# Optimization experiments

Measured on AMD Instinct MI355X. Metric: run time of the kernel, lower is better.

## Reference

```python
import jax, jax.numpy as jnp
import numpy as np

T, B, D = 4096, 64, 64
SCALE = D ** (-0.5)


def setup_inputs() -> dict:
    key = jax.random.key(0)
    ks = jax.random.split(key, 8)
    init = 1.0 / np.sqrt(D)  # mimic nn.Linear default scale roughly
    return {
        "eeg": jax.random.normal(ks[0], (T, B, D), dtype=jnp.float32),
        "fnirs": jax.random.normal(ks[1], (T, B, D), dtype=jnp.float32),
        "Wq": jax.random.normal(ks[2], (D, D), dtype=jnp.float32) * init,
        "bq": jax.random.normal(ks[3], (D,), dtype=jnp.float32) * init,
        "Wk": jax.random.normal(ks[4], (D, D), dtype=jnp.float32) * init,
        "bk": jax.random.normal(ks[5], (D,), dtype=jnp.float32) * init,
        "Wv": jax.random.normal(ks[6], (D, D), dtype=jnp.float32) * init,
        "bv": jax.random.normal(ks[7], (D,), dtype=jnp.float32) * init,
    }


def reference(eeg, fnirs, Wq, bq, Wk, bk, Wv, bv):
    # Linear layers: x @ W.T + b (torch nn.Linear convention, W is [out, in])
    q = jnp.einsum("tbd,od->tbo", eeg, Wq) + bq      # [T, B, D]
    k = jnp.einsum("tbd,od->tbo", fnirs, Wk) + bk    # [T, B, D]
    v = jnp.einsum("tbd,od->tbo", fnirs, Wv) + bv    # [T, B, D]
    # Elementwise QK gating score, summed over feature dim -> [T, B, 1]
    score = jnp.sum(q * k, axis=-1, keepdims=True) * SCALE
    # Softmax over the sequence axis (dim=0)
    attn = jax.nn.softmax(score, axis=0)
    # Residual combine
    return eeg + attn * v
```

## Files before the change

### kernel.cpp

```cpp
#include <hip/hip_runtime.h>
#include <hip/hip_bf16.h>
#include <math.h>

#define T_DIM 4096
#define B_DIM 64
#define NROWS (T_DIM * B_DIM)
#define NTILES (NROWS / 16)

#define WS_MFRAG 0
#define WS_VFRAG 2048
#define WS_U     4096
#define WS_W     4160
#define WS_C     4224
#define WS_MX    4240
#define WS_INV   4304
#define WS_PM    4368
#define WS_PS    8464
#define WS_SCORE 16384

typedef __attribute__((ext_vector_type(4))) float f32x4;
typedef __attribute__((ext_vector_type(8))) short bf16x8;

static __device__ inline short f2bf(float x) {
  __hip_bfloat16 h = __float2bfloat16(x);
  return *reinterpret_cast<short*>(&h);
}

static __device__ inline bf16x8 cvt8(const float4 a, const float4 b) {
  bf16x8 r;
  r[0] = f2bf(a.x); r[1] = f2bf(a.y); r[2] = f2bf(a.z); r[3] = f2bf(a.w);
  r[4] = f2bf(b.x); r[5] = f2bf(b.y); r[6] = f2bf(b.z); r[7] = f2bf(b.w);
  return r;
}

static __device__ inline float dot4(const float4 a, const float4 b, float acc) {
  acc = fmaf(a.x, b.x, acc); acc = fmaf(a.y, b.y, acc);
  acc = fmaf(a.z, b.z, acc); acc = fmaf(a.w, b.w, acc);
  return acc;
}

static __device__ __host__ inline int frag_idx(int d, int k) {
  return ((d >> 4) * 2 + (k >> 5)) * 512 +
         ((((k >> 3) & 3) * 16 + (d & 15)) * 8) + (k & 7);
}

static __device__ inline void gll16(const float* src, float* ldsbase) {
  __builtin_amdgcn_global_load_lds(
      (const __attribute__((address_space(1))) unsigned int*)src,
      (__attribute__((address_space(3))) unsigned int*)ldsbase, 16, 0, 0);
}

__global__ __launch_bounds__(64) void k1_precompute(
    const float* __restrict__ Wq, const float* __restrict__ bq,
    const float* __restrict__ Wk, const float* __restrict__ bk,
    const float* __restrict__ Wv, float* __restrict__ ws) {
  const int tid = threadIdx.x;
  const int blk = blockIdx.x;
  unsigned short* __restrict__ mfrag = (unsigned short*)(ws + WS_MFRAG);
  unsigned short* __restrict__ vfrag = (unsigned short*)(ws + WS_VFRAG);
  if (blk < 64) {
    const int d = blk;
    float acc = 0.f;
#pragma unroll
    for (int o = 0; o < 64; ++o)
      acc = fmaf(Wq[o * 64 + d], Wk[o * 64 + tid], acc);
    const int idx = frag_idx(d, tid);
    mfrag[idx] = (unsigned short)f2bf(acc);
    vfrag[idx] = (unsigned short)f2bf(Wv[d * 64 + tid]);
  } else {
    float uacc = 0.f, wacc = 0.f, cacc = 0.f;
#pragma unroll
    for (int o = 0; o < 64; ++o) {
      uacc = fmaf(bq[o], Wk[o * 64 + tid], uacc);
      wacc = fmaf(Wq[o * 64 + tid], bk[o], wacc);
      cacc = fmaf(bq[o], bk[o], cacc);
    }
    ws[WS_U + tid] = uacc;
    ws[WS_W + tid] = wacc;
    if (tid == 0) ws[WS_C] = cacc;
  }
}


#define K2_STAGE(b_, t_)                                                      \
  {                                                                           \
    const size_t rb_ = (size_t)(t_) * 16;                                     \
    float* Lb_ = &stg[wv][b_][0];                                             \
    _Pragma("unroll") for (int q = 0; q < 4; ++q)                             \
        gll16(fnirs + (rb_ + (lane & 15)) * 64 + (q * 4 + (lane >> 4)) * 4,   \
              Lb_ + q * 256);                                                 \
    _Pragma("unroll") for (int q = 0; q < 4; ++q)                             \
        gll16(eeg + (rb_ + (lane & 15)) * 64 + (q * 4 + (lane >> 4)) * 4,     \
              Lb_ + 1024 + q * 256);                                          \
  }

#define K2_COMP(b_, t_)                                                       \
  {                                                                           \
    const float* LF_ = &stg[wv][b_][0];                                       \
    const float* LE_ = &stg[wv][b_][1024];                                    \
    const float4 f0a_ = *reinterpret_cast<const float4*>(LF_ + (2 * g) * 64 + c * 4); \
    const float4 f0b_ = *reinterpret_cast<const float4*>(LF_ + (2 * g + 1) * 64 + c * 4); \
    const float4 f1a_ = *reinterpret_cast<const float4*>(LF_ + (8 + 2 * g) * 64 + c * 4); \
    const float4 f1b_ = *reinterpret_cast<const float4*>(LF_ + (9 + 2 * g) * 64 + c * 4); \
    float s_ = dot4(f0a_, u0a, dot4(f0b_, u0b, dot4(f1a_, u1a, dot4(f1b_, u1b, 0.f)))); \
    const bf16x8 a0_ = cvt8(f0a_, f0b_);                                      \
    const bf16x8 a1_ = cvt8(f1a_, f1b_);                                      \
    f32x4 acc_[4];                                                            \
    _Pragma("unroll") for (int dt = 0; dt < 4; ++dt) {                        \
      acc_[dt] = __builtin_amdgcn_mfma_f32_16x16x32_bf16(bm[dt][0], a0_, zero, 0, 0, 0); \
      acc_[dt] = __builtin_amdgcn_mfma_f32_16x16x32_bf16(bm[dt][1], a1_, acc_[dt], 0, 0, 0); \
    }                                                                         \
    _Pragma("unroll") for (int dt = 0; dt < 4; ++dt) {                        \
      const float4 Ed_ = *reinterpret_cast<const float4*>(LE_ + (dt * 4 + g) * 64 + c * 4); \
      float4 h_;                                                              \
      h_.x = acc_[dt][0] + wfr[dt].x; h_.y = acc_[dt][1] + wfr[dt].y;         \
      h_.z = acc_[dt][2] + wfr[dt].z; h_.w = acc_[dt][3] + wfr[dt].w;         \
      s_ = dot4(Ed_, h_, s_);                                                 \
    }                                                                         \
    s_ += __shfl_xor(s_, 16, 64);                                             \
    s_ += __shfl_xor(s_, 32, 64);                                             \
    if (lane < 16) score[(t_) * 16 + lane] = (s_ + cb) * 0.125f;              \
  }

__global__ __launch_bounds__(256, 2) void k2_score_mfma(
    const float* __restrict__ eeg, const float* __restrict__ fnirs,
    const float* __restrict__ wsf, float* __restrict__ score) {
  __shared__ float stg[4][2][2048];
  __shared__ unsigned short mw[4096];
  __shared__ float wl[64];

  const int tid = threadIdx.x;
  const int lane = tid & 63;
  const int wv = tid >> 6;
  const int c = lane & 15;
  const int g = lane >> 4;

  {
    const float4* msrc = reinterpret_cast<const float4*>(wsf + WS_MFRAG);
    float4* mdst = reinterpret_cast<float4*>(mw);
    mdst[tid] = msrc[tid];
    mdst[tid + 256] = msrc[tid + 256];
    if (tid < 64) wl[tid] = wsf[WS_W + tid];
  }
  __syncthreads();

  bf16x8 bm[4][2];
#pragma unroll
  for (int dt = 0; dt < 4; ++dt)
#pragma unroll
    for (int kf = 0; kf < 2; ++kf)
      bm[dt][kf] = *reinterpret_cast<const bf16x8*>(
          mw + (((dt * 2 + kf) << 9) + lane * 8));
  float4 wfr[4];
#pragma unroll
  for (int dt = 0; dt < 4; ++dt)
    wfr[dt] = *reinterpret_cast<const float4*>(&wl[dt * 16 + g * 4]);
  const float4 u0a = *reinterpret_cast<const float4*>(wsf + WS_U + g * 8);
  const float4 u0b = *reinterpret_cast<const float4*>(wsf + WS_U + g * 8 + 4);
  const float4 u1a = *reinterpret_cast<const float4*>(wsf + WS_U + 32 + g * 8);
  const float4 u1b = *reinterpret_cast<const float4*>(wsf + WS_U + 36 + g * 8);
  const float cb = wsf[WS_C];
  const f32x4 zero = {0.f, 0.f, 0.f, 0.f};

  const int t0 = (blockIdx.x * 4 + wv) * 4;

  K2_STAGE(0, t0);
  K2_STAGE(1, t0 + 1);
  asm volatile("s_waitcnt vmcnt(8)" ::: "memory");
  __builtin_amdgcn_sched_barrier(0);
  K2_COMP(0, t0);
  K2_STAGE(0, t0 + 2);
  asm volatile("s_waitcnt vmcnt(8)" ::: "memory");
  __builtin_amdgcn_sched_barrier(0);
  K2_COMP(1, t0 + 1);
  K2_STAGE(1, t0 + 3);
  asm volatile("s_waitcnt vmcnt(8)" ::: "memory");
  __builtin_amdgcn_sched_barrier(0);
  K2_COMP(0, t0 + 2);
  asm volatile("s_waitcnt vmcnt(0)" ::: "memory");
  __builtin_amdgcn_sched_barrier(0);
  K2_COMP(1, t0 + 3);
}

__global__ __launch_bounds__(256) void k3a_partial(
    const float* __restrict__ sc, float* __restrict__ pm,
    float* __restrict__ ps) {
  __shared__ float sm[4][64], ss[4][64];
  const int tid = threadIdx.x;
  const int b = tid & 63;
  const int tq = tid >> 6;
  const int t0 = blockIdx.x * 64;
  float m = -1e30f, s = 0.f;
#pragma unroll
  for (int k = 0; k < 16; ++k) {
    const float v = sc[(size_t)(t0 + k * 4 + tq) * 64 + b];
    const float mn = fmaxf(m, v);
    s = s * __expf(m - mn) + __expf(v - mn);
    m = mn;
  }
  sm[tq][b] = m; ss[tq][b] = s;
  __syncthreads();
  if (tid < 64) {
    float M = sm[0][b], S = ss[0][b];
#pragma unroll
    for (int w = 1; w < 4; ++w) {
      const float m2 = sm[w][b], s2 = ss[w][b];
      const float Mn = fmaxf(M, m2);
      S = S * __expf(M - Mn) + s2 * __expf(m2 - Mn);
      M = Mn;
    }
    pm[blockIdx.x * 64 + b] = M;
    ps[blockIdx.x * 64 + b] = S;
  }
}

__global__ __launch_bounds__(64) void k3b_combine(
    const float* __restrict__ pm, const float* __restrict__ ps,
    float* __restrict__ mx, float* __restrict__ inv) {
  const int b = threadIdx.x;
  float M = pm[b], S = ps[b];
#pragma unroll
  for (int ck = 1; ck < 64; ++ck) {
    const float m2 = pm[ck * 64 + b], s2 = ps[ck * 64 + b];
    const float Mn = fmaxf(M, m2);
    S = S * __expf(M - Mn) + s2 * __expf(m2 - Mn);
    M = Mn;
  }
  mx[b] = M;
  inv[b] = 1.0f / S;
}


#define K4_STAGE(b_, t_, scv_)                                                \
  {                                                                           \
    const size_t rb_ = (size_t)(t_) * 16;                                     \
    float* Lb_ = &stg[wv][b_][0];                                             \
    _Pragma("unroll") for (int q = 0; q < 4; ++q)                             \
        gll16(fnirs + (rb_ + (lane & 15)) * 64 + (q * 4 + (lane >> 4)) * 4,   \
              Lb_ + q * 256);                                                 \
    _Pragma("unroll") for (int q = 0; q < 4; ++q)                             \
        gll16(eeg + (rb_ + (lane & 15)) * 64 + (q * 4 + (lane >> 4)) * 4,     \
              Lb_ + 1024 + q * 256);                                          \
    scv_ = score[(t_) * 16 + c];                                              \
  }

#define K4_COMP(b_, t_, scv_)                                                 \
  {                                                                           \
    const float* LF_ = &stg[wv][b_][0];                                       \
    const float* LE_ = &stg[wv][b_][1024];                                    \
    const float4 f0a_ = *reinterpret_cast<const float4*>(LF_ + (2 * g) * 64 + c * 4); \
    const float4 f0b_ = *reinterpret_cast<const float4*>(LF_ + (2 * g + 1) * 64 + c * 4); \
    const float4 f1a_ = *reinterpret_cast<const float4*>(LF_ + (8 + 2 * g) * 64 + c * 4); \
    const float4 f1b_ = *reinterpret_cast<const float4*>(LF_ + (9 + 2 * g) * 64 + c * 4); \
    const bf16x8 a0_ = cvt8(f0a_, f0b_);                                      \
    const bf16x8 a1_ = cvt8(f1a_, f1b_);                                      \
    f32x4 acc_[4];                                                            \
    _Pragma("unroll") for (int dt = 0; dt < 4; ++dt) {                        \
      acc_[dt] = __builtin_amdgcn_mfma_f32_16x16x32_bf16(bm[dt][0], a0_, zero, 0, 0, 0); \
      acc_[dt] = __builtin_amdgcn_mfma_f32_16x16x32_bf16(bm[dt][1], a1_, acc_[dt], 0, 0, 0); \
    }                                                                         \
    const int bl_ = (((t_) * 16) & 63) + c;                                   \
    const float aC_ = __expf((scv_) - mxl[bl_]) * invl[bl_];                  \
    float* ob_ = out + ((size_t)(t_) * 16 + c) * 64;                          \
    _Pragma("unroll") for (int dt = 0; dt < 4; ++dt) {                        \
      const float4 Ed_ = *reinterpret_cast<const float4*>(LE_ + (dt * 4 + g) * 64 + c * 4); \
      float4 o_;                                                              \
      o_.x = fmaf(aC_, acc_[dt][0] + bvf[dt].x, Ed_.x);                       \
      o_.y = fmaf(aC_, acc_[dt][1] + bvf[dt].y, Ed_.y);                       \
      o_.z = fmaf(aC_, acc_[dt][2] + bvf[dt].z, Ed_.z);                       \
      o_.w = fmaf(aC_, acc_[dt][3] + bvf[dt].w, Ed_.w);                       \
      *reinterpret_cast<float4*>(ob_ + dt * 16 + g * 4) = o_;                 \
    }                                                                         \
  }

__global__ __launch_bounds__(256, 2) void k4_output_mfma(
    const float* __restrict__ eeg, const float* __restrict__ fnirs,
    const float* __restrict__ wsf, const float* __restrict__ bv,
    const float* __restrict__ score, float* __restrict__ out) {
  __shared__ float stg[4][2][2048];
  __shared__ unsigned short vw[4096];
  __shared__ float bvl[64], mxl[64], invl[64];

  const int tid = threadIdx.x;
  const int lane = tid & 63;
  const int wv = tid >> 6;
  const int c = lane & 15;
  const int g = lane >> 4;

  {
    const float4* vsrc = reinterpret_cast<const float4*>(wsf + WS_VFRAG);
    float4* vdst = reinterpret_cast<float4*>(vw);
    vdst[tid] = vsrc[tid];
    vdst[tid + 256] = vsrc[tid + 256];
    if (tid < 64) {
      bvl[tid] = bv[tid];
      mxl[tid] = wsf[WS_MX + tid];
      invl[tid] = wsf[WS_INV + tid];
    }
  }
  __syncthreads();

  bf16x8 bm[4][2];
#pragma unroll
  for (int dt = 0; dt < 4; ++dt)
#pragma unroll
    for (int kf = 0; kf < 2; ++kf)
      bm[dt][kf] = *reinterpret_cast<const bf16x8*>(
          vw + (((dt * 2 + kf) << 9) + lane * 8));
  float4 bvf[4];
#pragma unroll
  for (int dt = 0; dt < 4; ++dt)
    bvf[dt] = *reinterpret_cast<const float4*>(&bvl[dt * 16 + g * 4]);
  const f32x4 zero = {0.f, 0.f, 0.f, 0.f};

  const int t0 = (blockIdx.x * 4 + wv) * 4;
  float scA, scB;

  K4_STAGE(0, t0, scA);
  K4_STAGE(1, t0 + 1, scB);
  asm volatile("s_waitcnt vmcnt(9)" ::: "memory");
  __builtin_amdgcn_sched_barrier(0);
  K4_COMP(0, t0, scA);
  K4_STAGE(0, t0 + 2, scA);
  asm volatile("s_waitcnt vmcnt(9)" ::: "memory");
  __builtin_amdgcn_sched_barrier(0);
  K4_COMP(1, t0 + 1, scB);
  K4_STAGE(1, t0 + 3, scB);
  asm volatile("s_waitcnt vmcnt(9)" ::: "memory");
  __builtin_amdgcn_sched_barrier(0);
  K4_COMP(0, t0 + 2, scA);
  asm volatile("s_waitcnt vmcnt(0)" ::: "memory");
  __builtin_amdgcn_sched_barrier(0);
  K4_COMP(1, t0 + 3, scB);
}

extern "C" void kernel_launch(void* const* d_in, const int* in_sizes, int n_in,
                              void* d_out, int out_size, void* d_ws, size_t ws_size,
                              hipStream_t stream) {
  const float* eeg   = (const float*)d_in[0];
  const float* fnirs = (const float*)d_in[1];
  const float* Wq    = (const float*)d_in[2];
  const float* bq    = (const float*)d_in[3];
  const float* Wk    = (const float*)d_in[4];
  const float* bk    = (const float*)d_in[5];
  const float* Wv    = (const float*)d_in[6];
  const float* bv    = (const float*)d_in[7];
  float* out = (float*)d_out;
  float* ws  = (float*)d_ws;

  k1_precompute<<<65, 64, 0, stream>>>(Wq, bq, Wk, bk, Wv, ws);
  k2_score_mfma<<<NTILES / 16, 256, 0, stream>>>(eeg, fnirs, ws, ws + WS_SCORE);
  k3a_partial<<<64, 256, 0, stream>>>(ws + WS_SCORE, ws + WS_PM, ws + WS_PS);
  k3b_combine<<<1, 64, 0, stream>>>(ws + WS_PM, ws + WS_PS,
                                    ws + WS_MX, ws + WS_INV);
  k4_output_mfma<<<NTILES / 16, 256, 0, stream>>>(eeg, fnirs, ws, bv,
                                                  ws + WS_SCORE, out);
}
```

Measured before the change: 70.90 us.

## Fuse score, softmax stats, and output into one cooperative persistent kernel

Replaces the four kernels (score, two-stage softmax reduction, output) with one cooperative kernel of 256 blocks that uses grid syncs between phases. Each wave now handles 16 tiles in a longer double-buffered loop instead of 4. The softmax statistics are computed by 64 blocks, one per batch column, with a two-pass max-then-sum block reduction. The aim is to remove launch gaps and the extra partial-reduction pass, at the cost of grid-sync latency, fewer blocks to spread across CUs, and a three-launch fallback when cooperative launch is unavailable.

```diff
diff --git a/kernel.cpp b/kernel.cpp
--- a/kernel.cpp
+++ b/kernel.cpp
@@ -1,11 +1,16 @@
 #include <hip/hip_runtime.h>
 #include <hip/hip_bf16.h>
+#include <hip/hip_cooperative_groups.h>
 #include <math.h>
+
+namespace cg = cooperative_groups;
 
 #define T_DIM 4096
 #define B_DIM 64
 #define NROWS (T_DIM * B_DIM)
 #define NTILES (NROWS / 16)
+#define NBLK 256
+#define TPW 16
 
 #define WS_MFRAG 0
 #define WS_VFRAG 2048
@@ -14,8 +19,6 @@
 #define WS_C     4224
 #define WS_MX    4240
 #define WS_INV   4304
-#define WS_PM    4368
-#define WS_PS    8464
 #define WS_SCORE 16384
 
 typedef __attribute__((ext_vector_type(4))) float f32x4;
@@ -82,7 +85,7 @@
 }
 
 
-#define K2_STAGE(b_, t_)                                                      \
+#define P1_STAGE(b_, t_)                                                      \
   {                                                                           \
     const size_t rb_ = (size_t)(t_) * 16;                                     \
     float* Lb_ = &stg[wv][b_][0];                                             \
@@ -94,7 +97,7 @@
               Lb_ + 1024 + q * 256);                                          \
   }
 
-#define K2_COMP(b_, t_)                                                       \
+#define P1_COMP(b_, t_)                                                       \
   {                                                                           \
     const float* LF_ = &stg[wv][b_][0];                                       \
     const float* LE_ = &stg[wv][b_][1024];                                    \
@@ -122,116 +125,7 @@
     if (lane < 16) score[(t_) * 16 + lane] = (s_ + cb) * 0.125f;              \
   }
 
-__global__ __launch_bounds__(256, 2) void k2_score_mfma(
-    const float* __restrict__ eeg, const float* __restrict__ fnirs,
-    const float* __restrict__ wsf, float* __restrict__ score) {
-  __shared__ float stg[4][2][2048];
-  __shared__ unsigned short mw[4096];
-  __shared__ float wl[64];
-
-  const int tid = threadIdx.x;
-  const int lane = tid & 63;
-  const int wv = tid >> 6;
-  const int c = lane & 15;
-  const int g = lane >> 4;
-
-  {
-    const float4* msrc = reinterpret_cast<const float4*>(wsf + WS_MFRAG);
-    float4* mdst = reinterpret_cast<float4*>(mw);
-    mdst[tid] = msrc[tid];
-    mdst[tid + 256] = msrc[tid + 256];
-    if (tid < 64) wl[tid] = wsf[WS_W + tid];
-  }
-  __syncthreads();
-
-  bf16x8 bm[4][2];
-#pragma unroll
-  for (int dt = 0; dt < 4; ++dt)
-#pragma unroll
-    for (int kf = 0; kf < 2; ++kf)
-      bm[dt][kf] = *reinterpret_cast<const bf16x8*>(
-          mw + (((dt * 2 + kf) << 9) + lane * 8));
-  float4 wfr[4];
-#pragma unroll
-  for (int dt = 0; dt < 4; ++dt)
-    wfr[dt] = *reinterpret_cast<const float4*>(&wl[dt * 16 + g * 4]);
-  const float4 u0a = *reinterpret_cast<const float4*>(wsf + WS_U + g * 8);
-  const float4 u0b = *reinterpret_cast<const float4*>(wsf + WS_U + g * 8 + 4);
-  const float4 u1a = *reinterpret_cast<const float4*>(wsf + WS_U + 32 + g * 8);
-  const float4 u1b = *reinterpret_cast<const float4*>(wsf + WS_U + 36 + g * 8);
-  const float cb = wsf[WS_C];
-  const f32x4 zero = {0.f, 0.f, 0.f, 0.f};
-
-  const int t0 = (blockIdx.x * 4 + wv) * 4;
-
-  K2_STAGE(0, t0);
-  K2_STAGE(1, t0 + 1);
-  asm volatile("s_waitcnt vmcnt(8)" ::: "memory");
-  __builtin_amdgcn_sched_barrier(0);
-  K2_COMP(0, t0);
-  K2_STAGE(0, t0 + 2);
-  asm volatile("s_waitcnt vmcnt(8)" ::: "memory");
-  __builtin_amdgcn_sched_barrier(0);
-  K2_COMP(1, t0 + 1);
-  K2_STAGE(1, t0 + 3);
-  asm volatile("s_waitcnt vmcnt(8)" ::: "memory");
-  __builtin_amdgcn_sched_barrier(0);
-  K2_COMP(0, t0 + 2);
-  asm volatile("s_waitcnt vmcnt(0)" ::: "memory");
-  __builtin_amdgcn_sched_barrier(0);
-  K2_COMP(1, t0 + 3);
-}
-
-__global__ __launch_bounds__(256) void k3a_partial(
-    const float* __restrict__ sc, float* __restrict__ pm,
-    float* __restrict__ ps) {
-  __shared__ float sm[4][64], ss[4][64];
-  const int tid = threadIdx.x;
-  const int b = tid & 63;
-  const int tq = tid >> 6;
-  const int t0 = blockIdx.x * 64;
-  float m = -1e30f, s = 0.f;
-#pragma unroll
-  for (int k = 0; k < 16; ++k) {
-    const float v = sc[(size_t)(t0 + k * 4 + tq) * 64 + b];
-    const float mn = fmaxf(m, v);
-    s = s * __expf(m - mn) + __expf(v - mn);
-    m = mn;
-  }
-  sm[tq][b] = m; ss[tq][b] = s;
-  __syncthreads();
-  if (tid < 64) {
-    float M = sm[0][b], S = ss[0][b];
-#pragma unroll
-    for (int w = 1; w < 4; ++w) {
-      const float m2 = sm[w][b], s2 = ss[w][b];
-      const float Mn = fmaxf(M, m2);
-      S = S * __expf(M - Mn) + s2 * __expf(m2 - Mn);
-      M = Mn;
-    }
-    pm[blockIdx.x * 64 + b] = M;
-    ps[blockIdx.x * 64 + b] = S;
-  }
-}
-
-__global__ __launch_bounds__(64) void k3b_combine(
-    const float* __restrict__ pm, const float* __restrict__ ps,
-    float* __restrict__ mx, float* __restrict__ inv) {
-  const int b = threadIdx.x;
-  float M = pm[b], S = ps[b];
-#pragma unroll
-  for (int ck = 1; ck < 64; ++ck) {
-    const float m2 = pm[ck * 64 + b], s2 = ps[ck * 64 + b];
-    const float Mn = fmaxf(M, m2);
-    S = S * __expf(M - Mn) + s2 * __expf(m2 - Mn);
-    M = Mn;
-  }
-  mx[b] = M;
-  inv[b] = 1.0f / S;
-}
-
-
-#define K4_STAGE(b_, t_, scv_)                                                \
+#define P3_STAGE(b_, t_, scv_)                                                \
   {                                                                           \
     const size_t rb_ = (size_t)(t_) * 16;                                     \
     float* Lb_ = &stg[wv][b_][0];                                             \
@@ -244,7 +138,7 @@
     scv_ = score[(t_) * 16 + c];                                              \
   }
 
-#define K4_COMP(b_, t_, scv_)                                                 \
+#define P3_COMP(b_, t_, scv_)                                                 \
   {                                                                           \
     const float* LF_ = &stg[wv][b_][0];                                       \
     const float* LE_ = &stg[wv][b_][1024];                                    \
@@ -273,65 +167,158 @@
     }                                                                         \
   }
 
-__global__ __launch_bounds__(256, 2) void k4_output_mfma(
+#define VMWAIT(n)                                                             \
+  asm volatile("s_waitcnt vmcnt(" #n ")" ::: "memory");                       \
+  __builtin_amdgcn_sched_barrier(0);
+
+template <int MODE>
+__global__ __launch_bounds__(256, 2) void fused_all(
     const float* __restrict__ eeg, const float* __restrict__ fnirs,
-    const float* __restrict__ wsf, const float* __restrict__ bv,
-    const float* __restrict__ score, float* __restrict__ out) {
+    float* __restrict__ wsf, const float* __restrict__ bv,
+    float* __restrict__ out) {
   __shared__ float stg[4][2][2048];
-  __shared__ unsigned short vw[4096];
-  __shared__ float bvl[64], mxl[64], invl[64];
+  __shared__ unsigned short wfrag[4096];
+  __shared__ float vec64[64];
+  __shared__ float mxl[64], invl[64];
+  __shared__ float red[8];
 
   const int tid = threadIdx.x;
   const int lane = tid & 63;
   const int wv = tid >> 6;
   const int c = lane & 15;
   const int g = lane >> 4;
-
-  {
-    const float4* vsrc = reinterpret_cast<const float4*>(wsf + WS_VFRAG);
-    float4* vdst = reinterpret_cast<float4*>(vw);
-    vdst[tid] = vsrc[tid];
-    vdst[tid + 256] = vsrc[tid + 256];
-    if (tid < 64) {
-      bvl[tid] = bv[tid];
-      mxl[tid] = wsf[WS_MX + tid];
-      invl[tid] = wsf[WS_INV + tid];
-    }
-  }
-  __syncthreads();
-
-  bf16x8 bm[4][2];
-#pragma unroll
-  for (int dt = 0; dt < 4; ++dt)
-#pragma unroll
-    for (int kf = 0; kf < 2; ++kf)
-      bm[dt][kf] = *reinterpret_cast<const bf16x8*>(
-          vw + (((dt * 2 + kf) << 9) + lane * 8));
-  float4 bvf[4];
-#pragma unroll
-  for (int dt = 0; dt < 4; ++dt)
-    bvf[dt] = *reinterpret_cast<const float4*>(&bvl[dt * 16 + g * 4]);
+  float* __restrict__ score = wsf + WS_SCORE;
   const f32x4 zero = {0.f, 0.f, 0.f, 0.f};
-
-  const int t0 = (blockIdx.x * 4 + wv) * 4;
-  float scA, scB;
-
-  K4_STAGE(0, t0, scA);
-  K4_STAGE(1, t0 + 1, scB);
-  asm volatile("s_waitcnt vmcnt(9)" ::: "memory");
-  __builtin_amdgcn_sched_barrier(0);
-  K4_COMP(0, t0, scA);
-  K4_STAGE(0, t0 + 2, scA);
-  asm volatile("s_waitcnt vmcnt(9)" ::: "memory");
-  __builtin_amdgcn_sched_barrier(0);
-  K4_COMP(1, t0 + 1, scB);
-  K4_STAGE(1, t0 + 3, scB);
-  asm volatile("s_waitcnt vmcnt(9)" ::: "memory");
-  __builtin_amdgcn_sched_barrier(0);
-  K4_COMP(0, t0 + 2, scA);
-  asm volatile("s_waitcnt vmcnt(0)" ::: "memory");
-  __builtin_amdgcn_sched_barrier(0);
-  K4_COMP(1, t0 + 3, scB);
+  const int t0 = (blockIdx.x * 4 + wv) * TPW;
+
+  if (MODE & 1) {
+    {
+      const float4* msrc = reinterpret_cast<const float4*>(wsf + WS_MFRAG);
+      float4* mdst = reinterpret_cast<float4*>(wfrag);
+      mdst[tid] = msrc[tid];
+      mdst[tid + 256] = msrc[tid + 256];
+      if (tid < 64) vec64[tid] = wsf[WS_W + tid];
+    }
+    __syncthreads();
+
+    bf16x8 bm[4][2];
+#pragma unroll
+    for (int dt = 0; dt < 4; ++dt)
+#pragma unroll
+      for (int kf = 0; kf < 2; ++kf)
+        bm[dt][kf] = *reinterpret_cast<const bf16x8*>(
+            wfrag + (((dt * 2 + kf) << 9) + lane * 8));
+    float4 wfr[4];
+#pragma unroll
+    for (int dt = 0; dt < 4; ++dt)
+      wfr[dt] = *reinterpret_cast<const float4*>(&vec64[dt * 16 + g * 4]);
+    const float4 u0a = *reinterpret_cast<const float4*>(wsf + WS_U + g * 8);
+    const float4 u0b = *reinterpret_cast<const float4*>(wsf + WS_U + g * 8 + 4);
+    const float4 u1a = *reinterpret_cast<const float4*>(wsf + WS_U + 32 + g * 8);
+    const float4 u1b = *reinterpret_cast<const float4*>(wsf + WS_U + 36 + g * 8);
+    const float cb = wsf[WS_C];
+
+    P1_STAGE(0, t0);
+    P1_STAGE(1, t0 + 1);
+#pragma unroll
+    for (int ii = 0; ii < 7; ++ii) {
+      VMWAIT(8);
+      P1_COMP(0, t0 + 2 * ii);
+      P1_STAGE(0, t0 + 2 * ii + 2);
+      VMWAIT(8);
+      P1_COMP(1, t0 + 2 * ii + 1);
+      P1_STAGE(1, t0 + 2 * ii + 3);
+    }
+    VMWAIT(8);
+    P1_COMP(0, t0 + 14);
+    VMWAIT(0);
+    P1_COMP(1, t0 + 15);
+  }
+
+  if constexpr (MODE == 7) {
+    __threadfence();
+    cg::this_grid().sync();
+  }
+
+  if (MODE & 2) {
+    if (blockIdx.x < 64) {
+      const int b = blockIdx.x;
+      float vals[16];
+      float m = -1e30f;
+#pragma unroll
+      for (int k = 0; k < 16; ++k) {
+        vals[k] = score[(size_t)(k * 256 + tid) * 64 + b];
+        m = fmaxf(m, vals[k]);
+      }
+#pragma unroll
+      for (int off = 32; off > 0; off >>= 1)
+        m = fmaxf(m, __shfl_xor(m, off, 64));
+      if ((tid & 63) == 0) red[tid >> 6] = m;
+      __syncthreads();
+      m = fmaxf(fmaxf(red[0], red[1]), fmaxf(red[2], red[3]));
+      float s = 0.f;
+#pragma unroll
+      for (int k = 0; k < 16; ++k) s += __expf(vals[k] - m);
+#pragma unroll
+      for (int off = 32; off > 0; off >>= 1)
+        s += __shfl_xor(s, off, 64);
+      if ((tid & 63) == 0) red[4 + (tid >> 6)] = s;
+      __syncthreads();
+      if (tid == 0) {
+        wsf[WS_MX + b] = m;
+        wsf[WS_INV + b] = 1.0f / (red[4] + red[5] + red[6] + red[7]);
+      }
+    }
+  }
+
+  if constexpr (MODE == 7) {
+    __threadfence();
+    cg::this_grid().sync();
+  }
+
+  if (MODE & 4) {
+    {
+      const float4* vsrc = reinterpret_cast<const float4*>(wsf + WS_VFRAG);
+      float4* vdst = reinterpret_cast<float4*>(wfrag);
+      vdst[tid] = vsrc[tid];
+      vdst[tid + 256] = vsrc[tid + 256];
+      if (tid < 64) {
+        vec64[tid] = bv[tid];
+        mxl[tid] = wsf[WS_MX + tid];
+        invl[tid] = wsf[WS_INV + tid];
+      }
+    }
+    __syncthreads();
+
+    bf16x8 bm[4][2];
+#pragma unroll
+    for (int dt = 0; dt < 4; ++dt)
+#pragma unroll
+      for (int kf = 0; kf < 2; ++kf)
+        bm[dt][kf] = *reinterpret_cast<const bf16x8*>(
+            wfrag + (((dt * 2 + kf) << 9) + lane * 8));
+    float4 bvf[4];
+#pragma unroll
+    for (int dt = 0; dt < 4; ++dt)
+      bvf[dt] = *reinterpret_cast<const float4*>(&vec64[dt * 16 + g * 4]);
+
+    float scA, scB;
+    P3_STAGE(0, t0, scA);
+    P3_STAGE(1, t0 + 1, scB);
+#pragma unroll
+    for (int ii = 0; ii < 7; ++ii) {
+      VMWAIT(9);
+      P3_COMP(0, t0 + 2 * ii, scA);
+      P3_STAGE(0, t0 + 2 * ii + 2, scA);
+      VMWAIT(9);
+      P3_COMP(1, t0 + 2 * ii + 1, scB);
+      P3_STAGE(1, t0 + 2 * ii + 3, scB);
+    }
+    VMWAIT(9);
+    P3_COMP(0, t0 + 14, scA);
+    VMWAIT(0);
+    P3_COMP(1, t0 + 15, scB);
+  }
 }
 
 extern "C" void kernel_launch(void* const* d_in, const int* in_sizes, int n_in,
@@ -349,10 +336,23 @@
   float* ws  = (float*)d_ws;
 
   k1_precompute<<<65, 64, 0, stream>>>(Wq, bq, Wk, bk, Wv, ws);
-  k2_score_mfma<<<NTILES / 16, 256, 0, stream>>>(eeg, fnirs, ws, ws + WS_SCORE);
-  k3a_partial<<<64, 256, 0, stream>>>(ws + WS_SCORE, ws + WS_PM, ws + WS_PS);
-  k3b_combine<<<1, 64, 0, stream>>>(ws + WS_PM, ws + WS_PS,
-                                    ws + WS_MX, ws + WS_INV);
-  k4_output_mfma<<<NTILES / 16, 256, 0, stream>>>(eeg, fnirs, ws, bv,
-                                                  ws + WS_SCORE, out);
-}
+
+  int dev = 0;
+  (void)hipGetDevice(&dev);
+  int coop = 0;
+  (void)hipDeviceGetAttribute(&coop, hipDeviceAttributeCooperativeLaunch, dev);
+
+  hipError_t cerr = hipErrorUnknown;
+  if (coop) {
+    void* args[] = {(void*)&eeg, (void*)&fnirs, (void*)&ws, (void*)&bv,
+                    (void*)&out};
+    cerr = hipLaunchCooperativeKernel(
+        reinterpret_cast<void*>(&fused_all<7>), dim3(NBLK), dim3(256), args, 0,
+        stream);
+  }
+  if (cerr != hipSuccess) {
+    fused_all<1><<<NBLK, 256, 0, stream>>>(eeg, fnirs, ws, bv, out);
+    fused_all<2><<<64, 256, 0, stream>>>(eeg, fnirs, ws, bv, out);
+    fused_all<4><<<NBLK, 256, 0, stream>>>(eeg, fnirs, ws, bv, out);
+  }
+}
```

Result: slower. 217.6 us (+206.9%).
